# Optimization experiments

Measured on AMD Instinct MI355X. Metric: run time of the kernel, lower is better.

The kernel has to match this reference:

```python
import jax, jax.numpy as jnp
import numpy as np

B, S, E, H = 2, 2048, 1024, 16
DH = E // H  # 64


def setup_inputs() -> dict:
    key = jax.random.key(0)
    ks = jax.random.split(key, 5)
    scale = 1.0 / np.sqrt(E)
    x = jax.random.normal(ks[0], (B, S, E), dtype=jnp.float32)
    # stacked per-head kqv Linear weights: out = x @ Wkqv[h] + bkqv[h], producing (k, q, v) chunks
    Wkqv = jax.random.normal(ks[1], (H, E, 3 * DH), dtype=jnp.float32) * scale
    bkqv = jax.random.normal(ks[2], (H, 3 * DH), dtype=jnp.float32) * scale
    Wo = jax.random.normal(ks[3], (E, E), dtype=jnp.float32) * scale
    bo = jax.random.normal(ks[4], (E,), dtype=jnp.float32) * scale
    return {"x": x, "Wkqv": Wkqv, "bkqv": bkqv, "Wo": Wo, "bo": bo}


def reference(x, Wkqv, bkqv, Wo, bo):
    b, s, e = x.shape
    h, _, f = Wkqv.shape
    dh = f // 3
    # per-head projection, fused over heads: [b, h, s, 3*dh]
    kqv = jnp.einsum('bse,hef->bhsf', x, Wkqv) + bkqv[None, :, None, :]
    # chunk order in the original is k, q, v
    k, q, v = jnp.split(kqv, 3, axis=-1)
    scores = jnp.einsum('bhqd,bhkd->bhqk', q, k) / jnp.sqrt(jnp.asarray(dh, x.dtype))
    causal = jnp.tril(jnp.ones((s, s), dtype=bool))  # slice of the tril buffer
    scores = jnp.where(causal[None, None], scores, -jnp.inf)
    weights = jax.nn.softmax(scores, axis=-1)
    sa = jnp.einsum('bhqk,bhkd->bhqd', weights, v)
    # concat heads along feature dim (head order preserved)
    sa = sa.transpose(0, 2, 1, 3).reshape(b, s, h * dh)
    return sa @ Wo + bo
```

## Files before the change

### kernel.cpp

```cpp
#include <hip/hip_runtime.h>
#include <hip/hip_bf16.h>

typedef __attribute__((ext_vector_type(8))) short bf16x8;
typedef __attribute__((ext_vector_type(4))) float f32x4;
typedef unsigned short u16;

#define NEG_INF (-__builtin_inff())

__device__ __forceinline__ void gload16(const void* g, void* l) {
  __builtin_amdgcn_global_load_lds(
      (const __attribute__((address_space(1))) void*)g,
      (__attribute__((address_space(3))) void*)l, 16, 0, 0);
}

__device__ __forceinline__ u16 f2b(float f) {
  union { float f; unsigned u; } v;
  v.f = f;
  unsigned r = v.u + 0x7fff + ((v.u >> 16) & 1);
  return (u16)(r >> 16);
}

__global__ __launch_bounds__(256) void cvt_f2b_kernel(
    const float* __restrict__ in, u16* __restrict__ out, int n4) {
  int i = blockIdx.x * 256 + threadIdx.x;
  if (i >= n4) return;
  float4 v = ((const float4*)in)[i];
  ushort2 a = {f2b(v.x), f2b(v.y)}, b = {f2b(v.z), f2b(v.w)};
  ((ushort2*)out)[i * 2] = a;
  ((ushort2*)out)[i * 2 + 1] = b;
}

__global__ __launch_bounds__(256) void transpose_f2b(
    const float* __restrict__ src, u16* __restrict__ dst, int R, int C) {
  __shared__ u16 t[32][33];
  int c0 = blockIdx.x * 32, r0 = blockIdx.y * 32;
  const float* s = src + (size_t)blockIdx.z * R * C;
  u16* d = dst + (size_t)blockIdx.z * R * C;
  for (int i = threadIdx.y; i < 32; i += 8)
    t[i][threadIdx.x] = f2b(s[(size_t)(r0 + i) * C + c0 + threadIdx.x]);
  __syncthreads();
  for (int i = threadIdx.y; i < 32; i += 8)
    d[(size_t)(c0 + i) * R + r0 + threadIdx.x] = t[threadIdx.x][i];
}

__device__ __forceinline__ void gemm_mainloop_128(
    const __hip_bfloat16* __restrict__ A, const __hip_bfloat16* __restrict__ Bt,
    int K, int m0, int n0, f32x4 acc[4][4], char* AsB, char* BsB) {
  const int tid = threadIdx.x;
  const int wave = tid >> 6, lane = tid & 63;
  const int lhi = lane >> 4, llo = lane & 15;
  const int wr = wave >> 1, wc = wave & 1;
  f32x4 z = {0.f, 0.f, 0.f, 0.f};
#pragma unroll
  for (int i = 0; i < 4; i++)
#pragma unroll
    for (int j = 0; j < 4; j++) acc[i][j] = z;

  for (int k0 = 0; k0 < K; k0 += 32) {
    __syncthreads();
#pragma unroll
    for (int i = 0; i < 2; i++) {
      int qb = i * 256 + wave * 64;
      int q = qb + lane;
      gload16(A + ((size_t)(m0 + (q >> 2)) * K + k0 + (q & 3) * 8), AsB + qb * 16);
      gload16(Bt + ((size_t)(n0 + (q >> 2)) * K + k0 + (q & 3) * 8), BsB + qb * 16);
    }
    __syncthreads();
    bf16x8 a[4], b[4];
#pragma unroll
    for (int m4 = 0; m4 < 4; m4++)
      a[m4] = *(const bf16x8*)(AsB + (wr * 64 + m4 * 16 + llo) * 64 + lhi * 16);
#pragma unroll
    for (int n4 = 0; n4 < 4; n4++)
      b[n4] = *(const bf16x8*)(BsB + (wc * 64 + n4 * 16 + llo) * 64 + lhi * 16);
#pragma unroll
    for (int m4 = 0; m4 < 4; m4++)
#pragma unroll
      for (int n4 = 0; n4 < 4; n4++)
        acc[m4][n4] =
            __builtin_amdgcn_mfma_f32_16x16x32_bf16(a[m4], b[n4], acc[m4][n4], 0, 0, 0);
  }
}

__global__ __launch_bounds__(256) void kqv_gemm(
    const __hip_bfloat16* __restrict__ x, const __hip_bfloat16* __restrict__ WT,
    const float* __restrict__ bkqv, __hip_bfloat16* __restrict__ Qb,
    __hip_bfloat16* __restrict__ Kb, __hip_bfloat16* __restrict__ Vt) {
  __shared__ __align__(16) __hip_bfloat16 As[128 * 32];
  __shared__ __align__(16) __hip_bfloat16 Bs[128 * 32];
  const int m0 = blockIdx.y * 128, n0 = blockIdx.x * 128;
  f32x4 acc[4][4];
  gemm_mainloop_128(x, WT, 1024, m0, n0, acc, (char*)As, (char*)Bs);

  const int tid = threadIdx.x, wave = tid >> 6, lane = tid & 63;
  const int lhi = lane >> 4, llo = lane & 15;
  const int wr = wave >> 1, wc = wave & 1;
#pragma unroll
  for (int m4 = 0; m4 < 4; m4++)
#pragma unroll
    for (int n4 = 0; n4 < 4; n4++)
#pragma unroll
      for (int r = 0; r < 4; r++) {
        int mg = m0 + wr * 64 + m4 * 16 + lhi * 4 + r;
        int ng = n0 + wc * 64 + n4 * 16 + llo;
        int b = mg >> 11, s = mg & 2047;
        int h = ng / 192, f = ng % 192;
        float v = acc[m4][n4][r] + bkqv[h * 192 + f];
        int chunk = f >> 6, d = f & 63;
        size_t bh = (size_t)(b * 16 + h);
        if (chunk == 0)
          Kb[(bh * 2048 + s) * 64 + d] = __float2bfloat16(v);
        else if (chunk == 1)
          Qb[(bh * 2048 + s) * 64 + d] = __float2bfloat16(v * 0.180336880f);
        else
          Vt[(bh * 64 + d) * 2048 + s] = __float2bfloat16(v);
      }
}

__global__ __launch_bounds__(256) void attn_kernel(
    const __hip_bfloat16* __restrict__ Qb, const __hip_bfloat16* __restrict__ Kb,
    const __hip_bfloat16* __restrict__ Vt, __hip_bfloat16* __restrict__ SA) {
  __shared__ __align__(16) char lds[40960];
  const int bx0 = blockIdx.x;
  const int bx = (bx0 & 7) * 64 + (bx0 >> 3);
  const int bh = bx >> 4;
  const int ip = bx & 15;
  const int qa = 31 - ip, qbt = ip;
  const int nta = qa + 1, nt = nta + qbt + 1;
  const int b = bh >> 4, h = bh & 15;
  const int tid = threadIdx.x, wave = tid >> 6, lane = tid & 63;
  const int lhi = lane >> 4, llo = lane & 15;
  const int lhi4 = lhi * 4;

  const __hip_bfloat16* qpA =
      Qb + ((size_t)bh * 2048 + qa * 64 + wave * 16 + llo) * 64 + lhi * 8;
  const __hip_bfloat16* qpB =
      Qb + ((size_t)bh * 2048 + qbt * 64 + wave * 16 + llo) * 64 + lhi * 8;
  bf16x8 qA0 = *(const bf16x8*)qpA, qA1 = *(const bf16x8*)(qpA + 32);
  bf16x8 qB0 = *(const bf16x8*)qpB, qB1 = *(const bf16x8*)(qpB + 32);
  bf16x8 q0 = qA0, q1 = qA1;

  const char* Kg = (const char*)(Kb + (size_t)bh * 2048 * 64);
  const char* Vg = (const char*)(Vt + (size_t)bh * 64 * 2048);
  char* PsB = lds + 32768 + wave * 2048;

  f32x4 z = {0.f, 0.f, 0.f, 0.f};
  f32x4 o[4];
  float m_s = NEG_INF, l_s = 0.f;
#pragma unroll
  for (int i = 0; i < 4; i++) o[i] = z;
  int qg = qa * 64 + wave * 16 + llo;
  int qg0 = qa * 64 + wave * 16 + lhi4;

#define STAGE(c, k0)                                                          \
  {                                                                           \
    char* KsW = lds + (c)*8192;                                               \
    char* VsW = lds + 16384 + (c)*8192;                                       \
    _Pragma("unroll") for (int i = 0; i < 2; i++) {                           \
      int ch = i * 256 + tid;                                                 \
      int soff = (ch * 16) ^ (((ch >> 3) & 7) << 4);                          \
      gload16(Kg + (size_t)(k0)*128 + soff, KsW + (i * 256 + wave * 64) * 16);\
      int dd = ch >> 3, c8 = ch & 7;                                          \
      int boff = (c8 * 16) ^ ((dd & 7) << 4);                                 \
      gload16(Vg + (size_t)dd * 4096 + (size_t)(k0)*2 + boff,                 \
              VsW + (i * 256 + wave * 64) * 16);                              \
    }                                                                         \
  }

  STAGE(0, 0);
  int cur = 0;

  for (int T = 0; T < nt; T++) {
    const int Tn = T + 1;
    if (Tn < nt) {
      const int k0n = (Tn < nta ? Tn : Tn - nta) * 64;
      STAGE(cur ^ 1, k0n);
      asm volatile("s_waitcnt vmcnt(4)" ::: "memory");
    } else {
      asm volatile("s_waitcnt vmcnt(0)" ::: "memory");
    }
    __builtin_amdgcn_s_barrier();
    __builtin_amdgcn_sched_barrier(0);

    const int k0 = (T < nta ? T : T - nta) * 64;
    const bool masked = (T == nta - 1) || (T == nt - 1);
    const char* KsB = lds + cur * 8192;
    const char* VsB = lds + 16384 + cur * 8192;

    f32x4 s[4] = {z, z, z, z};
#pragma unroll
    for (int j = 0; j < 4; j++) {
      const int row = j * 16 + llo;
      const int rx = (row & 7) << 4;
      bf16x8 bk0 = *(const bf16x8*)(KsB + ((row * 128 + lhi * 16) ^ rx));
      bf16x8 bk1 = *(const bf16x8*)(KsB + ((row * 128 + 64 + lhi * 16) ^ rx));
      s[j] = __builtin_amdgcn_mfma_f32_16x16x32_bf16(bk0, q0, s[j], 0, 0, 0);
      s[j] = __builtin_amdgcn_mfma_f32_16x16x32_bf16(bk1, q1, s[j], 0, 0, 0);
    }

    if (masked) {
#pragma unroll
      for (int j = 0; j < 4; j++)
#pragma unroll
        for (int r = 0; r < 4; r++)
          if (k0 + j * 16 + lhi4 + r > qg) s[j][r] = NEG_INF;
    }
    float pmax = s[0][0];
#pragma unroll
    for (int j = 0; j < 4; j++)
#pragma unroll
      for (int r = 0; r < 4; r++) pmax = fmaxf(pmax, s[j][r]);
    pmax = fmaxf(pmax, __shfl_xor(pmax, 16));
    pmax = fmaxf(pmax, __shfl_xor(pmax, 32));
    if (!__all(pmax - m_s <= 5.0f)) {
      const float mn = fmaxf(m_s, pmax);
      const float sc = __builtin_exp2f(m_s - mn);
      m_s = mn;
      l_s *= sc;
#pragma unroll
      for (int r = 0; r < 4; r++) {
        const float scr = __shfl(sc, lhi4 + r);
#pragma unroll
        for (int n4 = 0; n4 < 4; n4++) o[n4][r] *= scr;
      }
    }
    const int px = (llo & 7) << 4;
    float ps = 0.f;
#pragma unroll
    for (int j = 0; j < 4; j++) {
      ushort4 pw;
#pragma unroll
      for (int r = 0; r < 4; r++) {
        const float p = __builtin_exp2f(s[j][r] - m_s);
        ps += p;
        ((__hip_bfloat16*)&pw)[r] = __float2bfloat16(p);
      }
      *(ushort4*)(PsB + ((llo * 128 + j * 32 + lhi * 8) ^ px)) = pw;
    }
    l_s += ps;

    {
      bf16x8 ap0 = *(const bf16x8*)(PsB + ((llo * 128 + lhi * 16) ^ px));
      bf16x8 ap1 = *(const bf16x8*)(PsB + ((llo * 128 + 64 + lhi * 16) ^ px));
#pragma unroll
      for (int n4 = 0; n4 < 4; n4++) {
        const int d = n4 * 16 + llo;
        const int dx = (d & 7) << 4;
        bf16x8 bv0 = *(const bf16x8*)(VsB + ((d * 128 + lhi * 16) ^ dx));
        bf16x8 bv1 = *(const bf16x8*)(VsB + ((d * 128 + 64 + lhi * 16) ^ dx));
        o[n4] = __builtin_amdgcn_mfma_f32_16x16x32_bf16(ap0, bv0, o[n4], 0, 0, 0);
        o[n4] = __builtin_amdgcn_mfma_f32_16x16x32_bf16(ap1, bv1, o[n4], 0, 0, 0);
      }
    }
    __builtin_amdgcn_sched_barrier(0);
    __builtin_amdgcn_s_barrier();

    if (T == nta - 1) {
      float l = l_s;
      l += __shfl_xor(l, 16);
      l += __shfl_xor(l, 32);
      const float inv = 1.f / l;
#pragma unroll
      for (int r = 0; r < 4; r++) {
        const float invr = __shfl(inv, lhi4 + r);
        const size_t ob = ((size_t)b * 2048 + qg0 + r) * 1024 + h * 64;
#pragma unroll
        for (int n4 = 0; n4 < 4; n4++)
          SA[ob + n4 * 16 + llo] = __float2bfloat16(o[n4][r] * invr);
      }
#pragma unroll
      for (int i = 0; i < 4; i++) o[i] = z;
      m_s = NEG_INF;
      l_s = 0.f;
      q0 = qB0; q1 = qB1;
      qg = qbt * 64 + wave * 16 + llo;
      qg0 = qbt * 64 + wave * 16 + lhi4;
    }
    cur ^= 1;
  }

  {
    float l = l_s;
    l += __shfl_xor(l, 16);
    l += __shfl_xor(l, 32);
    const float inv = 1.f / l;
#pragma unroll
    for (int r = 0; r < 4; r++) {
      const float invr = __shfl(inv, lhi4 + r);
      const size_t ob = ((size_t)b * 2048 + qg0 + r) * 1024 + h * 64;
#pragma unroll
      for (int n4 = 0; n4 < 4; n4++)
        SA[ob + n4 * 16 + llo] = __float2bfloat16(o[n4][r] * invr);
    }
  }
#undef STAGE
}

__global__ __launch_bounds__(256) void out_gemm(
    const __hip_bfloat16* __restrict__ SA, const __hip_bfloat16* __restrict__ WoT,
    const float* __restrict__ bo, float* __restrict__ out) {
  __shared__ __align__(16) __hip_bfloat16 As[128 * 32];
  __shared__ __align__(16) __hip_bfloat16 Bs[128 * 32];
  const int m0 = blockIdx.y * 128, n0 = blockIdx.x * 128;
  f32x4 acc[4][4];
  gemm_mainloop_128(SA, WoT, 1024, m0, n0, acc, (char*)As, (char*)Bs);

  const int tid = threadIdx.x, wave = tid >> 6, lane = tid & 63;
  const int lhi = lane >> 4, llo = lane & 15;
  const int wr = wave >> 1, wc = wave & 1;
#pragma unroll
  for (int m4 = 0; m4 < 4; m4++)
#pragma unroll
    for (int n4 = 0; n4 < 4; n4++)
#pragma unroll
      for (int r = 0; r < 4; r++) {
        int mg = m0 + wr * 64 + m4 * 16 + lhi * 4 + r;
        int ng = n0 + wc * 64 + n4 * 16 + llo;
        out[(size_t)mg * 1024 + ng] = acc[m4][n4][r] + bo[ng];
      }
}

extern "C" void kernel_launch(void* const* d_in, const int* in_sizes, int n_in,
                              void* d_out, int out_size, void* d_ws, size_t ws_size,
                              hipStream_t stream) {
  const float* x = (const float*)d_in[0];
  const float* Wkqv = (const float*)d_in[1];
  const float* bkqv = (const float*)d_in[2];
  const float* Wo = (const float*)d_in[3];
  const float* bo = (const float*)d_in[4];
  float* out = (float*)d_out;

  char* w = (char*)d_ws;
  __hip_bfloat16* WkqvT = (__hip_bfloat16*)(w);
  __hip_bfloat16* WoT = (__hip_bfloat16*)(w + 6291456);
  __hip_bfloat16* Qb = (__hip_bfloat16*)(w + 8388608);
  __hip_bfloat16* Kb = (__hip_bfloat16*)(w + 16777216);
  __hip_bfloat16* Vt = (__hip_bfloat16*)(w + 25165824);
  __hip_bfloat16* SAb = (__hip_bfloat16*)(w + 33554432);
  __hip_bfloat16* xb = (__hip_bfloat16*)(w + 41943040);

  cvt_f2b_kernel<<<4096, 256, 0, stream>>>(x, (u16*)xb, 1048576);
  transpose_f2b<<<dim3(6, 32, 16), dim3(32, 8, 1), 0, stream>>>(
      Wkqv, (u16*)WkqvT, 1024, 192);
  transpose_f2b<<<dim3(32, 32, 1), dim3(32, 8, 1), 0, stream>>>(
      Wo, (u16*)WoT, 1024, 1024);
  kqv_gemm<<<dim3(24, 32), 256, 0, stream>>>(xb, WkqvT, bkqv, Qb, Kb, Vt);
  attn_kernel<<<512, 256, 0, stream>>>(Qb, Kb, Vt, SAb);
  out_gemm<<<dim3(8, 32), 256, 0, stream>>>(SAb, WoT, bo, out);
}
```

Before: 129.1 us.

## Double-buffer LDS tiles in GEMM mainloop to overlap global loads with MFMA

Converts the shared GEMM mainloop used by the kqv and output projections into a two-stage pipeline. It issues the next K-slice's global-to-LDS loads before computing on the current buffer, with explicit vmcnt waits and barriers. This hides global memory latency behind MFMA work instead of stalling on every K step. It doubles LDS per block to 32KB, which may reduce occupancy, and relies on manual waitcnt accounting.

```diff
diff --git a/kernel.cpp b/kernel.cpp
--- a/kernel.cpp
+++ b/kernel.cpp
@@ -56,41 +56,64 @@
 #pragma unroll
     for (int j = 0; j < 4; j++) acc[i][j] = z;
 
-  for (int k0 = 0; k0 < K; k0 += 32) {
-    __syncthreads();
-#pragma unroll
-    for (int i = 0; i < 2; i++) {
-      int qb = i * 256 + wave * 64;
-      int q = qb + lane;
-      gload16(A + ((size_t)(m0 + (q >> 2)) * K + k0 + (q & 3) * 8), AsB + qb * 16);
-      gload16(Bt + ((size_t)(n0 + (q >> 2)) * K + k0 + (q & 3) * 8), BsB + qb * 16);
-    }
-    __syncthreads();
+#define GSTAGE(c, kk)                                                          \
+  {                                                                            \
+    char* AsW = AsB + (c)*8192;                                                \
+    char* BsW = BsB + (c)*8192;                                                \
+    _Pragma("unroll") for (int i = 0; i < 2; i++) {                            \
+      int cb = i * 256 + wave * 64;                                            \
+      int cq = cb + lane;                                                      \
+      gload16(A + ((size_t)(m0 + (cq >> 2)) * K + (kk) + (cq & 3) * 8),        \
+              AsW + cb * 16);                                                  \
+      gload16(Bt + ((size_t)(n0 + (cq >> 2)) * K + (kk) + (cq & 3) * 8),       \
+              BsW + cb * 16);                                                  \
+    }                                                                          \
+  }
+
+  GSTAGE(0, 0);
+  int cur = 0;
+  const int nk = K >> 5;
+  for (int t = 0; t < nk; t++) {
+    if (t + 1 < nk) {
+      GSTAGE(cur ^ 1, (t + 1) * 32);
+      asm volatile("s_waitcnt vmcnt(4)" ::: "memory");
+    } else {
+      asm volatile("s_waitcnt vmcnt(0)" ::: "memory");
+    }
+    __builtin_amdgcn_s_barrier();
+    __builtin_amdgcn_sched_barrier(0);
+
+    const char* Ar = AsB + cur * 8192;
+    const char* Br = BsB + cur * 8192;
     bf16x8 a[4], b[4];
 #pragma unroll
     for (int m4 = 0; m4 < 4; m4++)
-      a[m4] = *(const bf16x8*)(AsB + (wr * 64 + m4 * 16 + llo) * 64 + lhi * 16);
+      a[m4] = *(const bf16x8*)(Ar + (wr * 64 + m4 * 16 + llo) * 64 + lhi * 16);
 #pragma unroll
     for (int n4 = 0; n4 < 4; n4++)
-      b[n4] = *(const bf16x8*)(BsB + (wc * 64 + n4 * 16 + llo) * 64 + lhi * 16);
+      b[n4] = *(const bf16x8*)(Br + (wc * 64 + n4 * 16 + llo) * 64 + lhi * 16);
 #pragma unroll
     for (int m4 = 0; m4 < 4; m4++)
 #pragma unroll
       for (int n4 = 0; n4 < 4; n4++)
         acc[m4][n4] =
             __builtin_amdgcn_mfma_f32_16x16x32_bf16(a[m4], b[n4], acc[m4][n4], 0, 0, 0);
-  }
+    __builtin_amdgcn_sched_barrier(0);
+    __builtin_amdgcn_s_barrier();
+    cur ^= 1;
+  }
+#undef GSTAGE
 }
 
 __global__ __launch_bounds__(256) void kqv_gemm(
     const __hip_bfloat16* __restrict__ x, const __hip_bfloat16* __restrict__ WT,
     const float* __restrict__ bkqv, __hip_bfloat16* __restrict__ Qb,
     __hip_bfloat16* __restrict__ Kb, __hip_bfloat16* __restrict__ Vt) {
-  __shared__ __align__(16) __hip_bfloat16 As[128 * 32];
-  __shared__ __align__(16) __hip_bfloat16 Bs[128 * 32];
+  __shared__ __align__(16) char As[16384];
+  __shared__ __align__(16) char Bs[16384];
   const int m0 = blockIdx.y * 128, n0 = blockIdx.x * 128;
   f32x4 acc[4][4];
-  gemm_mainloop_128(x, WT, 1024, m0, n0, acc, (char*)As, (char*)Bs);
+  gemm_mainloop_128(x, WT, 1024, m0, n0, acc, As, Bs);
 
   const int tid = threadIdx.x, wave = tid >> 6, lane = tid & 63;
   const int lhi = lane >> 4, llo = lane & 15;
@@ -299,11 +322,11 @@
 __global__ __launch_bounds__(256) void out_gemm(
     const __hip_bfloat16* __restrict__ SA, const __hip_bfloat16* __restrict__ WoT,
     const float* __restrict__ bo, float* __restrict__ out) {
-  __shared__ __align__(16) __hip_bfloat16 As[128 * 32];
-  __shared__ __align__(16) __hip_bfloat16 Bs[128 * 32];
+  __shared__ __align__(16) char As[16384];
+  __shared__ __align__(16) char Bs[16384];
   const int m0 = blockIdx.y * 128, n0 = blockIdx.x * 128;
   f32x4 acc[4][4];
-  gemm_mainloop_128(SA, WoT, 1024, m0, n0, acc, (char*)As, (char*)Bs);
+  gemm_mainloop_128(SA, WoT, 1024, m0, n0, acc, As, Bs);
 
   const int tid = threadIdx.x, wave = tid >> 6, lane = tid & 63;
   const int lhi = lane >> 4, llo = lane & 15;
```

Result: no change. 130.2 us (+0.8%).
